# Kernel optimization log

Hardware: AMD Instinct MI355X
Metric: run time of the kernel (lower is better)

The kernel has to match this reference:

```python
import jax, jax.numpy as jnp
import numpy as np

B, H, S, D = 2, 16, 2048, 64

def setup_inputs() -> dict:
    key = jax.random.key(0)
    kq, kk, kv = jax.random.split(key, 3)
    Q = jax.random.normal(kq, (B, H, S, D), dtype=jnp.float32)
    K = jax.random.normal(kk, (B, H, S, D), dtype=jnp.float32)
    V = jax.random.normal(kv, (B, H, S, D), dtype=jnp.float32)
    # causal mask, broadcastable over batch/heads: True = attend
    mask = jnp.tril(jnp.ones((S, S), dtype=bool))[None, None, :, :]
    return {"Q": Q, "K": K, "V": V, "mask": mask}

def reference(Q, K, V, mask):
    d_k = Q.shape[-1]
    scale = 1.0 / jnp.sqrt(jnp.asarray(d_k, Q.dtype))
    # [..., q, k] scores; mask applied as -inf before softmax (matches torch.where)
    scores = jnp.einsum('bhqd,bhkd->bhqk', Q, K) * scale
    scores = jnp.where(mask, scores, -jnp.inf)
    weights = jax.nn.softmax(scores, axis=-1)
    out = jnp.einsum('bhqk,bhkd->bhqd', weights, V)
    return out
```

## Files before the change

### kernel.cpp

```cpp
#include <hip/hip_runtime.h>
#include <hip/hip_bf16.h>

#define S_LEN 2048
#define D_DIM 64
#define NBH   32
#define NE    (NBH * S_LEN * D_DIM)

typedef __attribute__((ext_vector_type(8))) short bf16x8;
typedef __attribute__((ext_vector_type(4))) short s16x4;
typedef __attribute__((ext_vector_type(2))) unsigned u32x2;
typedef __attribute__((ext_vector_type(4))) unsigned u32x4;
typedef __attribute__((ext_vector_type(4))) float f32x4;

__device__ __forceinline__ f32x4 mfma16(bf16x8 a, bf16x8 b, f32x4 c) {
  return __builtin_amdgcn_mfma_f32_16x16x32_bf16(a, b, c, 0, 0, 0);
}

__device__ __forceinline__ void gload16(const void* g, void* l) {
  __builtin_amdgcn_global_load_lds(
      (const __attribute__((address_space(1))) unsigned*)g,
      (__attribute__((address_space(3))) unsigned*)l, 16, 0, 0);
}

__device__ __forceinline__ unsigned cvtpk(float a, float b) {
  unsigned r;
  asm("v_cvt_pk_bf16_f32 %0, %1, %2" : "=v"(r) : "v"(a), "v"(b));
  return r;
}
__device__ __forceinline__ u32x2 split2(float a, float b) {
  u32x2 r;
  r.x = cvtpk(a, b);
  const float fa = __builtin_bit_cast(float, r.x << 16);
  const float fb = __builtin_bit_cast(float, r.x & 0xffff0000u);
  r.y = cvtpk(a - fa, b - fb);
  return r;
}

__global__ __launch_bounds__(256) void prepass(const float* __restrict__ K,
                                               const float* __restrict__ V,
                                               unsigned short* __restrict__ Kh,
                                               unsigned short* __restrict__ Kl,
                                               unsigned short* __restrict__ Vh,
                                               unsigned short* __restrict__ Vl) {
  __shared__ float t[64][65];
  const int tid = threadIdx.x;
  if (blockIdx.x < 2048) {
    const int i = ((int)blockIdx.x * 256 + tid) * 8;
    float4 v0 = *(const float4*)(K + i);
    float4 v1 = *(const float4*)(K + i + 4);
    u32x4 H, L;
    u32x2 s;
    s = split2(v0.x, v0.y); H[0] = s.x; L[0] = s.y;
    s = split2(v0.z, v0.w); H[1] = s.x; L[1] = s.y;
    s = split2(v1.x, v1.y); H[2] = s.x; L[2] = s.y;
    s = split2(v1.z, v1.w); H[3] = s.x; L[3] = s.y;
    *(u32x4*)(Kh + i) = H;
    *(u32x4*)(Kl + i) = L;
  } else {
    const int bid = (int)blockIdx.x - 2048;
    const int bh  = bid >> 5;
    const int kv0 = (bid & 31) << 6;
#pragma unroll
    for (int pp = 0; pp < 4; ++pp) {
      const int r  = (tid >> 4) + pp * 16;
      const int c4 = (tid & 15) << 2;
      float4 v = *(const float4*)(V + ((size_t)bh * S_LEN + kv0 + r) * D_DIM + c4);
      t[r][c4] = v.x; t[r][c4 + 1] = v.y; t[r][c4 + 2] = v.z; t[r][c4 + 3] = v.w;
    }
    __syncthreads();
    const int d  = tid >> 2;
    const int k0 = (tid & 3) << 4;
    u32x4 H0, L0, H1, L1;
#pragma unroll
    for (int jj = 0; jj < 4; ++jj) {
      u32x2 s = split2(t[k0 + 2 * jj][d], t[k0 + 2 * jj + 1][d]);
      H0[jj] = s.x; L0[jj] = s.y;
    }
#pragma unroll
    for (int jj = 0; jj < 4; ++jj) {
      u32x2 s = split2(t[k0 + 8 + 2 * jj][d], t[k0 + 9 + 2 * jj][d]);
      H1[jj] = s.x; L1[jj] = s.y;
    }
    const size_t ob = ((size_t)bh * D_DIM + d) * S_LEN + kv0 + k0;
    *(u32x4*)(Vh + ob)     = H0;
    *(u32x4*)(Vh + ob + 8) = H1;
    *(u32x4*)(Vl + ob)     = L0;
    *(u32x4*)(Vl + ob + 8) = L1;
  }
}

__global__ __launch_bounds__(256) void attn_main(const float* __restrict__ Q,
                                                 const unsigned short* __restrict__ Kh,
                                                 const unsigned short* __restrict__ Kl,
                                                 const unsigned short* __restrict__ Vh,
                                                 const unsigned short* __restrict__ Vl,
                                                 float* __restrict__ Out) {
  __shared__ __align__(16) char smem[40960];
  unsigned short* sKh = (unsigned short*)smem;
  unsigned short* sKl = (unsigned short*)(smem + 8192);
  unsigned short* sVh = (unsigned short*)(smem + 16384);
  unsigned short* sVl = (unsigned short*)(smem + 24576);
  short*          sPh = (short*)(smem + 32768);
  short*          sPl = (short*)(smem + 36864);

  const int tid   = threadIdx.x;
  const int bh    = blockIdx.x & 31;
  const int qt    = 31 - (blockIdx.x >> 5);
  const int qbase = qt << 6;
  const int wave  = tid >> 6;
  const int lane  = tid & 63;
  const int c     = lane & 15;
  const int g     = lane >> 4;
  const int qw    = qbase + (wave << 4);

  const size_t bhO = (size_t)bh * (S_LEN * D_DIM);

  const float SC = 0.125f * 1.44269504088896340736f;
  bf16x8 qh[2], ql[2];
#pragma unroll
  for (int ch = 0; ch < 2; ++ch) {
    const float* src = Q + bhO + (size_t)(qw + c) * D_DIM + ch * 32 + g * 8;
    float4 v0 = *(const float4*)src;
    float4 v1 = *(const float4*)(src + 4);
    float a[8] = {v0.x, v0.y, v0.z, v0.w, v1.x, v1.y, v1.z, v1.w};
    u32x4 H, L;
    u32x2 s;
    s = split2(a[0] * SC, a[1] * SC); H[0] = s.x; L[0] = s.y;
    s = split2(a[2] * SC, a[3] * SC); H[1] = s.x; L[1] = s.y;
    s = split2(a[4] * SC, a[5] * SC); H[2] = s.x; L[2] = s.y;
    s = split2(a[6] * SC, a[7] * SC); H[3] = s.x; L[3] = s.y;
    qh[ch] = __builtin_bit_cast(bf16x8, H);
    ql[ch] = __builtin_bit_cast(bf16x8, L);
  }

  f32x4 acc[4] = {{0.f,0.f,0.f,0.f},{0.f,0.f,0.f,0.f},{0.f,0.f,0.f,0.f},{0.f,0.f,0.f,0.f}};
  float m_r = -3.0e38f, l_r = 0.f;

  const unsigned short* gKh = Kh + bhO;
  const unsigned short* gKl = Kl + bhO;
  const unsigned short* gVh = Vh + bhO;
  const unsigned short* gVl = Vl + bhO;

  const int rs   = tid >> 3;
  const int kswz = ((tid & 7) ^ (rs & 7)) << 3;
  const int vrow = tid >> 2;
  const int vcol = (((tid & 3) ^ ((tid >> 3) & 3)) << 3);

  const int nIter = (qbase >> 5) + 2;

#define STAGE(itx, buf)                                                        \
  do {                                                                         \
    const int kv_ = (itx) << 5;                                                \
    gload16(gKh + (size_t)(kv_ + rs) * D_DIM + kswz,                           \
            sKh + ((buf) << 11) + (wave << 9));                                \
    gload16(gKl + (size_t)(kv_ + rs) * D_DIM + kswz,                           \
            sKl + ((buf) << 11) + (wave << 9));                                \
    gload16(gVh + (size_t)vrow * S_LEN + kv_ + vcol,                           \
            sVh + ((buf) << 11) + (wave << 9));                                \
    gload16(gVl + (size_t)vrow * S_LEN + kv_ + vcol,                           \
            sVl + ((buf) << 11) + (wave << 9));                                \
  } while (0)

  STAGE(0, 0);
  __syncthreads();
  int cur = 0;

  for (int it = 0; it < nIter; ++it) {
    if (it + 1 < nIter) STAGE(it + 1, cur ^ 1);
    const int kv0 = it << 5;

    if (kv0 <= qw + 15) {
      const int cb = cur << 11;
      f32x4 sj[2];
#pragma unroll
      for (int j = 0; j < 2; ++j) {
        const int row = (j << 4) + c;
        bf16x8 kfh[2], kfl[2];
#pragma unroll
        for (int ch = 0; ch < 2; ++ch) {
          const int p = ((ch << 2) + g) ^ (c & 7);
          kfh[ch] = *(const bf16x8*)&sKh[cb + (row << 6) + (p << 3)];
          kfl[ch] = *(const bf16x8*)&sKl[cb + (row << 6) + (p << 3)];
        }
        f32x4 sa = {0.f, 0.f, 0.f, 0.f};
        sa = mfma16(kfh[0], qh[0], sa);
        sa = mfma16(kfh[1], qh[1], sa);
        sa = mfma16(kfh[0], ql[0], sa);
        sa = mfma16(kfh[1], ql[1], sa);
        sa = mfma16(kfl[0], qh[0], sa);
        sa = mfma16(kfl[1], qh[1], sa);
        sj[j] = sa;
      }
      if (kv0 + 31 > qw) {
#pragma unroll
        for (int j = 0; j < 2; ++j) {
          const int kvb = kv0 + (j << 4) + (g << 2);
#pragma unroll
          for (int r = 0; r < 4; ++r) {
            if (kvb + r > qw + c) sj[j][r] = -3.0e38f;
          }
        }
      }
      float pm = fmaxf(fmaxf(fmaxf(sj[0][0], sj[0][1]), fmaxf(sj[0][2], sj[0][3])),
                       fmaxf(fmaxf(sj[1][0], sj[1][1]), fmaxf(sj[1][2], sj[1][3])));
      pm = fmaxf(pm, __shfl_xor(pm, 16));
      pm = fmaxf(pm, __shfl_xor(pm, 32));
      if (!__all(pm <= m_r)) {
        const float mn  = fmaxf(m_r, pm);
        const float fac = exp2f(m_r - mn);
        m_r = mn;
        l_r *= fac;
#pragma unroll
        for (int dt = 0; dt < 4; ++dt) acc[dt] *= fac;
      }
      float p[2][4];
      float ps = 0.f;
#pragma unroll
      for (int j = 0; j < 2; ++j)
#pragma unroll
        for (int r = 0; r < 4; ++r) {
          p[j][r] = exp2f(sj[j][r] - m_r);
          ps += p[j][r];
        }
      ps += __shfl_xor(ps, 16);
      ps += __shfl_xor(ps, 32);
      l_r += ps;

#pragma unroll
      for (int j = 0; j < 2; ++j) {
        u32x2 s0 = split2(p[j][0], p[j][1]);
        u32x2 s1 = split2(p[j][2], p[j][3]);
        const int blkp = ((j << 1) + (g >> 1)) ^ ((c >> 1) & 3);
        const int dw   = (wave << 8) + (c << 4) + (blkp << 2) + ((g & 1) << 1);
        u32x2 hw; hw[0] = s0.x; hw[1] = s1.x;
        u32x2 lw; lw[0] = s0.y; lw[1] = s1.y;
        *(s16x4*)&sPh[dw << 1] = __builtin_bit_cast(s16x4, hw);
        *(s16x4*)&sPl[dw << 1] = __builtin_bit_cast(s16x4, lw);
      }
      const int rdw = (wave << 8) + (c << 4) + ((g ^ ((c >> 1) & 3)) << 2);
      const bf16x8 pbh = *(const bf16x8*)&sPh[rdw << 1];
      const bf16x8 pbl = *(const bf16x8*)&sPl[rdw << 1];

#pragma unroll
      for (int dt = 0; dt < 4; ++dt) {
        const int vb = cb + (((dt << 4) + c) << 5) + ((g ^ ((c >> 1) & 3)) << 3);
        const bf16x8 vfh = *(const bf16x8*)&sVh[vb];
        const bf16x8 vfl = *(const bf16x8*)&sVl[vb];
        acc[dt] = mfma16(vfh, pbh, acc[dt]);
        acc[dt] = mfma16(vfl, pbh, acc[dt]);
        acc[dt] = mfma16(vfh, pbl, acc[dt]);
      }
    }
    __syncthreads();
    cur ^= 1;
  }

  const float inv = 1.0f / l_r;
  float (*ob)[68] = (float(*)[68])smem;
#pragma unroll
  for (int dt = 0; dt < 4; ++dt) {
    f32x4 o = acc[dt] * inv;
    *(f32x4*)&ob[(wave << 4) + c][(dt << 4) + (g << 2)] = o;
  }
  __syncthreads();
#pragma unroll
  for (int v = 0; v < 4; ++v) {
    const int row = (tid >> 4) + (v << 4);
    const int dc  = (tid & 15) << 2;
    float4 val = *(const float4*)&ob[row][dc];
    *(float4*)(Out + bhO + (size_t)(qbase + row) * D_DIM + dc) = val;
  }
}

extern "C" void kernel_launch(void* const* d_in, const int* in_sizes, int n_in,
                              void* d_out, int out_size, void* d_ws, size_t ws_size,
                              hipStream_t stream) {
  const float* Q = (const float*)d_in[0];
  const float* K = (const float*)d_in[1];
  const float* V = (const float*)d_in[2];

  unsigned short* Kh = (unsigned short*)d_ws;
  unsigned short* Kl = Kh + NE;
  unsigned short* Vh = Kl + NE;
  unsigned short* Vl = Vh + NE;
  float* Out = (float*)d_out;

  prepass<<<3072, 256, 0, stream>>>(K, V, Kh, Kl, Vh, Vl);
  attn_main<<<NBH * (S_LEN / 64), 256, 0, stream>>>(Q, Kh, Kl, Vh, Vl, Out);
}
```

Measured before the change: 188.7 us.

## Split KV range across two wave groups per block and merge softmax partials

Doubles the block to 512 threads: two groups of four waves each process half of the causal KV range for the same 64 query rows, each with its own double-buffered LDS staging. The partial accumulators, running max and sum are then merged through shared memory in a flash-decoding style combine. The aim is to shorten the long serial KV loop of the late query tiles and add more waves in flight. The cost is doubled LDS per block, which may lower occupancy, plus an extra merge step. It also adds a lazy rescale threshold (skip the rescale unless the max grows by more than 8).

```diff
diff --git a/kernel.cpp b/kernel.cpp
--- a/kernel.cpp
+++ b/kernel.cpp
@@ -89,29 +89,32 @@
   }
 }
 
-__global__ __launch_bounds__(256) void attn_main(const float* __restrict__ Q,
+__global__ __launch_bounds__(512) void attn_main(const float* __restrict__ Q,
                                                  const unsigned short* __restrict__ Kh,
                                                  const unsigned short* __restrict__ Kl,
                                                  const unsigned short* __restrict__ Vh,
                                                  const unsigned short* __restrict__ Vl,
                                                  float* __restrict__ Out) {
-  __shared__ __align__(16) char smem[40960];
+  __shared__ __align__(16) char smem[81920];
   unsigned short* sKh = (unsigned short*)smem;
-  unsigned short* sKl = (unsigned short*)(smem + 8192);
-  unsigned short* sVh = (unsigned short*)(smem + 16384);
-  unsigned short* sVl = (unsigned short*)(smem + 24576);
-  short*          sPh = (short*)(smem + 32768);
-  short*          sPl = (short*)(smem + 36864);
+  unsigned short* sKl = (unsigned short*)(smem + 16384);
+  unsigned short* sVh = (unsigned short*)(smem + 32768);
+  unsigned short* sVl = (unsigned short*)(smem + 49152);
+  short*          sPh = (short*)(smem + 65536);
+  short*          sPl = (short*)(smem + 73728);
 
   const int tid   = threadIdx.x;
   const int bh    = blockIdx.x & 31;
   const int qt    = 31 - (blockIdx.x >> 5);
   const int qbase = qt << 6;
   const int wave  = tid >> 6;
+  const int grp   = wave >> 2;
+  const int wsub  = wave & 3;
   const int lane  = tid & 63;
   const int c     = lane & 15;
   const int g     = lane >> 4;
-  const int qw    = qbase + (wave << 4);
+  const int qw    = qbase + (wsub << 4);
+  const int gtid  = tid & 255;
 
   const size_t bhO = (size_t)bh * (S_LEN * D_DIM);
 
@@ -141,36 +144,37 @@
   const unsigned short* gVh = Vh + bhO;
   const unsigned short* gVl = Vl + bhO;
 
-  const int rs   = tid >> 3;
-  const int kswz = ((tid & 7) ^ (rs & 7)) << 3;
-  const int vrow = tid >> 2;
-  const int vcol = (((tid & 3) ^ ((tid >> 3) & 3)) << 3);
-
-  const int nIter = (qbase >> 5) + 2;
+  const int rs   = gtid >> 3;
+  const int kswz = ((gtid & 7) ^ (rs & 7)) << 3;
+  const int vrow = gtid >> 2;
+  const int vcol = (((gtid & 3) ^ ((gtid >> 3) & 3)) << 3);
+
+  const int nIterT = (qbase >> 5) + 2;
+  const int nHalf  = (nIterT + 1) >> 1;
+  const int itStart = grp ? nHalf : 0;
+  const int itEnd   = grp ? nIterT : nHalf;
 
 #define STAGE(itx, buf)                                                        \
   do {                                                                         \
     const int kv_ = (itx) << 5;                                                \
-    gload16(gKh + (size_t)(kv_ + rs) * D_DIM + kswz,                           \
-            sKh + ((buf) << 11) + (wave << 9));                                \
-    gload16(gKl + (size_t)(kv_ + rs) * D_DIM + kswz,                           \
-            sKl + ((buf) << 11) + (wave << 9));                                \
-    gload16(gVh + (size_t)vrow * S_LEN + kv_ + vcol,                           \
-            sVh + ((buf) << 11) + (wave << 9));                                \
-    gload16(gVl + (size_t)vrow * S_LEN + kv_ + vcol,                           \
-            sVl + ((buf) << 11) + (wave << 9));                                \
+    const int rb_ = (((grp << 1) | (buf)) << 11) + (wsub << 9);                \
+    gload16(gKh + (size_t)(kv_ + rs) * D_DIM + kswz, sKh + rb_);               \
+    gload16(gKl + (size_t)(kv_ + rs) * D_DIM + kswz, sKl + rb_);               \
+    gload16(gVh + (size_t)vrow * S_LEN + kv_ + vcol, sVh + rb_);               \
+    gload16(gVl + (size_t)vrow * S_LEN + kv_ + vcol, sVl + rb_);               \
   } while (0)
 
-  STAGE(0, 0);
+  STAGE(itStart, 0);
   __syncthreads();
-  int cur = 0;
-
-  for (int it = 0; it < nIter; ++it) {
-    if (it + 1 < nIter) STAGE(it + 1, cur ^ 1);
-    const int kv0 = it << 5;
-
-    if (kv0 <= qw + 15) {
-      const int cb = cur << 11;
+
+  for (int il = 0; il < nHalf; ++il) {
+    const int myIt = itStart + il;
+    const bool act = myIt < itEnd;
+    if (act && myIt + 1 < itEnd) STAGE(myIt + 1, (il + 1) & 1);
+    const int kv0 = myIt << 5;
+
+    if (act && kv0 <= qw + 15) {
+      const int kb = ((grp << 1) | (il & 1)) << 11;
       f32x4 sj[2];
 #pragma unroll
       for (int j = 0; j < 2; ++j) {
@@ -179,8 +183,8 @@
 #pragma unroll
         for (int ch = 0; ch < 2; ++ch) {
           const int p = ((ch << 2) + g) ^ (c & 7);
-          kfh[ch] = *(const bf16x8*)&sKh[cb + (row << 6) + (p << 3)];
-          kfl[ch] = *(const bf16x8*)&sKl[cb + (row << 6) + (p << 3)];
+          kfh[ch] = *(const bf16x8*)&sKh[kb + (row << 6) + (p << 3)];
+          kfl[ch] = *(const bf16x8*)&sKl[kb + (row << 6) + (p << 3)];
         }
         f32x4 sa = {0.f, 0.f, 0.f, 0.f};
         sa = mfma16(kfh[0], qh[0], sa);
@@ -205,7 +209,7 @@
                        fmaxf(fmaxf(sj[1][0], sj[1][1]), fmaxf(sj[1][2], sj[1][3])));
       pm = fmaxf(pm, __shfl_xor(pm, 16));
       pm = fmaxf(pm, __shfl_xor(pm, 32));
-      if (!__all(pm <= m_r)) {
+      if (!__all(pm <= m_r + 8.0f)) {
         const float mn  = fmaxf(m_r, pm);
         const float fac = exp2f(m_r - mn);
         m_r = mn;
@@ -243,7 +247,7 @@
 
 #pragma unroll
       for (int dt = 0; dt < 4; ++dt) {
-        const int vb = cb + (((dt << 4) + c) << 5) + ((g ^ ((c >> 1) & 3)) << 3);
+        const int vb = kb + (((dt << 4) + c) << 5) + ((g ^ ((c >> 1) & 3)) << 3);
         const bf16x8 vfh = *(const bf16x8*)&sVh[vb];
         const bf16x8 vfl = *(const bf16x8*)&sVl[vb];
         acc[dt] = mfma16(vfh, pbh, acc[dt]);
@@ -252,23 +256,45 @@
       }
     }
     __syncthreads();
-    cur ^= 1;
-  }
-
-  const float inv = 1.0f / l_r;
-  float (*ob)[68] = (float(*)[68])smem;
-#pragma unroll
-  for (int dt = 0; dt < 4; ++dt) {
-    f32x4 o = acc[dt] * inv;
-    *(f32x4*)&ob[(wave << 4) + c][(dt << 4) + (g << 2)] = o;
+  }
+
+  float* ax = (float*)smem + wsub * 1040;
+  float* mf = (float*)(smem + 65536);
+  float* lf = mf + 64;
+  if (grp == 0) {
+#pragma unroll
+    for (int dt = 0; dt < 4; ++dt)
+#pragma unroll
+      for (int r = 0; r < 4; ++r)
+        ax[c * 65 + (dt << 4) + (g << 2) + r] = acc[dt][r];
+    if (g == 0) { mf[(wsub << 4) + c] = m_r; lf[(wsub << 4) + c] = l_r; }
   }
   __syncthreads();
-#pragma unroll
-  for (int v = 0; v < 4; ++v) {
-    const int row = (tid >> 4) + (v << 4);
-    const int dc  = (tid & 15) << 2;
-    float4 val = *(const float4*)&ob[row][dc];
-    *(float4*)(Out + bhO + (size_t)(qbase + row) * D_DIM + dc) = val;
+  float (*ob)[68] = (float(*)[68])(smem + 32768);
+  if (grp == 1) {
+    const float m0 = mf[(wsub << 4) + c], l0 = lf[(wsub << 4) + c];
+    const float M  = fmaxf(m0, m_r);
+    const float f0 = exp2f(m0 - M), f1 = exp2f(m_r - M);
+    const float inv = 1.0f / (f0 * l0 + f1 * l_r);
+#pragma unroll
+    for (int dt = 0; dt < 4; ++dt) {
+      f32x4 o;
+#pragma unroll
+      for (int r = 0; r < 4; ++r)
+        o[r] = (f0 * ax[c * 65 + (dt << 4) + (g << 2) + r] + f1 * acc[dt][r]) * inv;
+      *(f32x4*)&ob[(wsub << 4) + c][(dt << 4) + (g << 2)] = o;
+    }
+  }
+  __syncthreads();
+  if (grp == 1) {
+    const int t2 = tid & 255;
+#pragma unroll
+    for (int v = 0; v < 4; ++v) {
+      const int row = (t2 >> 4) + (v << 4);
+      const int dc  = (t2 & 15) << 2;
+      *(float4*)(Out + bhO + (size_t)(qbase + row) * D_DIM + dc) =
+          *(const float4*)&ob[row][dc];
+    }
   }
 }
 
@@ -286,5 +312,5 @@
   float* Out = (float*)d_out;
 
   prepass<<<3072, 256, 0, stream>>>(K, V, Kh, Kl, Vh, Vl);
-  attn_main<<<NBH * (S_LEN / 64), 256, 0, stream>>>(Q, Kh, Kl, Vh, Vl, Out);
-}
+  attn_main<<<NBH * (S_LEN / 64), 512, 0, stream>>>(Q, Kh, Kl, Vh, Vl, Out);
+}
```

Result: faster. 179.7 us (-4.8%).
